# Performance work log

Measured on AMD Instinct MI355X. Metric: run time of the kernel, lower is better.

Reference implementation:

```python
import jax, jax.numpy as jnp
import numpy as np

N_NODES = 100000
N_EDGES = 3200000
IN_DIM = 128
H_GCN = 64
H_LSTM = 64


def setup_inputs() -> dict:
    key = jax.random.key(0)
    ks = jax.random.split(key, 12)
    s = 0.05
    return {
        "x": jax.random.normal(ks[0], (IN_DIM, N_NODES), dtype=jnp.float32),
        "edge_index": jax.random.randint(ks[1], (2, N_EDGES), 0, N_NODES, dtype=jnp.int32),
        "W1": jax.random.normal(ks[2], (IN_DIM, H_GCN), dtype=jnp.float32) * s,
        "b1": jnp.zeros((H_GCN,), dtype=jnp.float32),
        "W2": jax.random.normal(ks[3], (H_GCN, H_GCN), dtype=jnp.float32) * s,
        "b2": jnp.zeros((H_GCN,), dtype=jnp.float32),
        "w_ih": jax.random.normal(ks[4], (4 * H_LSTM, H_GCN), dtype=jnp.float32) * s,
        "w_hh": jax.random.normal(ks[5], (4 * H_LSTM, H_LSTM), dtype=jnp.float32) * s,
        "b_ih": jax.random.normal(ks[6], (4 * H_LSTM,), dtype=jnp.float32) * s,
        "b_hh": jax.random.normal(ks[7], (4 * H_LSTM,), dtype=jnp.float32) * s,
        "fc_w": jax.random.normal(ks[8], (1, H_LSTM), dtype=jnp.float32) * s,
        "fc_b": jnp.zeros((1,), dtype=jnp.float32),
    }


def gcn_conv(x, src, dst, n, W, b):
    # PyG GCNConv: add self loops, symmetric norm D^-1/2 (A+I) D^-1/2, linear-first.
    h = x @ W  # [N, out]
    loop = jnp.arange(n, dtype=src.dtype)
    s = jnp.concatenate([src, loop])
    d = jnp.concatenate([dst, loop])
    deg = jax.ops.segment_sum(jnp.ones(d.shape, dtype=h.dtype), d, num_segments=n)
    dinv = jnp.where(deg > 0, jax.lax.rsqrt(deg), 0.0)
    norm = dinv[s] * dinv[d]  # [E+N]
    out = jax.ops.segment_sum(h[s] * norm[:, None], d, num_segments=n)
    return out + b


def reference(x, edge_index, W1, b1, W2, b2, w_ih, w_hh, b_ih, b_hh, fc_w, fc_b):
    xt = x.T  # data.x.T -> [N, input_dim]
    n = xt.shape[0]
    src, dst = edge_index[0], edge_index[1]
    h = jax.nn.relu(gcn_conv(xt, src, dst, n, W1, b1))
    h = gcn_conv(h, src, dst, n, W2, b2)
    z = h[0][None, :]  # [1, H_GCN] node 0 embedding
    # single-step LSTM, zero initial state (h0=c0=0)
    gates = z @ w_ih.T + b_ih + b_hh  # [1, 4H]
    i, f, g, o = jnp.split(gates, 4, axis=-1)
    c = jax.nn.sigmoid(i) * jnp.tanh(g)  # f*c0 = 0
    hy = jax.nn.sigmoid(o) * jnp.tanh(c)  # [1, H_LSTM]
    y = hy @ fc_w.T + fc_b  # [1, 1]
    return y[:, :, None]  # [1, 1, 1]
```

## Files before the change

### kernel.cpp

```cpp
#include <hip/hip_runtime.h>
#include <math.h>

#define N_NODES 100000
#define N_EDGES 3200000
#define IN_DIM 128
#define HG 64

#define E0CAP 2048
#define MCAP  65536
#define NBMW  3125
#define SCAN_BLOCKS 1024
#define BLK_E0 16

#define OFF_DEG       0u
#define OFF_SLOTMAP   400000u
#define OFF_CNT       800000u
#define OFF_ACC       800032u
#define OFF_BMS1      1324320u
#define OFF_BMNEED    1336864u
#define WS_ZERO_BYTES 1349408u
#define OFF_BCNT      1349408u
#define OFF_BLIST     1353504u
#define OFF_EDGES0    1419040u
#define OFF_SLOTNODE  1427232u
#define OFF_MLISTS    1435424u
#define OFF_MLISTD    1697568u

__device__ __forceinline__ float dinv_of(int degv) {
    return 1.0f / sqrtf((float)(degv + 1));
}

__global__ void k_scan0(const int* __restrict__ src, const int* __restrict__ dst,
                        int4* __restrict__ zbase, int* __restrict__ bcnt,
                        int* __restrict__ blist) {
    __shared__ int lcnt;
    __shared__ int lsrc[BLK_E0];
    if (threadIdx.x == 0) lcnt = 0;
    __syncthreads();
    int tid = blockIdx.x * blockDim.x + threadIdx.x;
    int nth = gridDim.x * blockDim.x;
    const int nz = WS_ZERO_BYTES / 16;
    int4 z; z.x = 0; z.y = 0; z.z = 0; z.w = 0;
    for (int i = tid; i < nz; i += nth) zbase[i] = z;
    const int4* dst4 = (const int4*)dst;
    const int n4 = N_EDGES / 4;
    for (int i = tid; i < n4; i += nth) {
        int4 dv = dst4[i];
        int ds[4] = {dv.x, dv.y, dv.z, dv.w};
#pragma unroll
        for (int k = 0; k < 4; k++) {
            if (ds[k] == 0) {
                int p = atomicAdd(&lcnt, 1);
                if (p < BLK_E0) lsrc[p] = src[4 * i + k];
            }
        }
    }
    __syncthreads();
    int c = lcnt; if (c > BLK_E0) c = BLK_E0;
    if (threadIdx.x == 0) bcnt[blockIdx.x] = c;
    for (int i = threadIdx.x; i < c; i += blockDim.x)
        blist[blockIdx.x * BLK_E0 + i] = lsrc[i];
}

__global__ void k_build_slots(const int* __restrict__ bcnt, const int* __restrict__ blist,
                              int* __restrict__ edges0, int* __restrict__ slotnodes,
                              int* __restrict__ slotmap, int* __restrict__ cnt,
                              unsigned* __restrict__ bmS1) {
    const int t = threadIdx.x;
    for (int b = t; b < SCAN_BLOCKS; b += blockDim.x) {
        int c = bcnt[b];
        if (c > 0) {
            int p = atomicAdd(&cnt[0], c);
            for (int j = 0; j < c && p + j < E0CAP; j++)
                edges0[p + j] = blist[b * BLK_E0 + j];
        }
    }
    __syncthreads();
    int n0 = atomicAdd(&cnt[0], 0); if (n0 > E0CAP) n0 = E0CAP;
    for (int i = t; i < n0 + 1; i += blockDim.x) {
        int s = (i == n0) ? 0 : edges0[i];
        if (atomicCAS(&slotmap[s], 0, 1) == 0) {
            int p = atomicAdd(&cnt[1], 1);
            if (p < E0CAP) slotnodes[p] = s;
        }
    }
    __syncthreads();
    int ns = atomicAdd(&cnt[1], 0); if (ns > E0CAP) ns = E0CAP;
    for (int i = t; i < ns; i += blockDim.x) {
        int s = slotnodes[i];
        slotmap[s] = i + 1;
        atomicOr(&bmS1[s >> 5], 1u << (s & 31));
    }
}

__global__ void k_match(const int* __restrict__ src, const int* __restrict__ dst,
                        const int* __restrict__ slotmap,
                        const unsigned* __restrict__ bmS1, unsigned* __restrict__ bmNeed,
                        int* __restrict__ cnt, int* __restrict__ mlistS,
                        int* __restrict__ mlistD) {
    __shared__ unsigned sbm[NBMW];
    for (int i = threadIdx.x; i < NBMW; i += blockDim.x) sbm[i] = bmS1[i];
    __syncthreads();
    int tid = blockIdx.x * blockDim.x + threadIdx.x;
    int nth = gridDim.x * blockDim.x;
    const int4* dst4 = (const int4*)dst;
    const int n4 = N_EDGES / 4;
    for (int i = tid; i < n4; i += nth) {
        int4 dv = dst4[i];
        unsigned ds[4] = {(unsigned)dv.x, (unsigned)dv.y, (unsigned)dv.z, (unsigned)dv.w};
#pragma unroll
        for (int k = 0; k < 4; k++) {
            unsigned d = ds[k];
            if ((sbm[d >> 5] >> (d & 31)) & 1u) {
                int e = 4 * i + k;
                int s = src[e];
                int sl = slotmap[d] - 1;
                int p = atomicAdd(&cnt[2], 1);
                if (p < MCAP) {
                    mlistS[p] = s | (sl << 17);
                    mlistD[p] = (int)d;
                }
                atomicOr(&bmNeed[s >> 5], 1u << (s & 31));
            }
        }
    }
}

__global__ void k_deg_need(const int* __restrict__ dst, const unsigned* __restrict__ bmS1,
                           const unsigned* __restrict__ bmNeed, int* __restrict__ deg) {
    __shared__ unsigned sbm[NBMW];
    for (int i = threadIdx.x; i < NBMW; i += blockDim.x) sbm[i] = bmS1[i] | bmNeed[i];
    __syncthreads();
    int tid = blockIdx.x * blockDim.x + threadIdx.x;
    int nth = gridDim.x * blockDim.x;
    const int4* dst4 = (const int4*)dst;
    const int n4 = N_EDGES / 4;
    for (int i = tid; i < n4; i += nth) {
        int4 dv = dst4[i];
        unsigned ds[4] = {(unsigned)dv.x, (unsigned)dv.y, (unsigned)dv.z, (unsigned)dv.w};
#pragma unroll
        for (int k = 0; k < 4; k++) {
            unsigned d = ds[k];
            if ((sbm[d >> 5] >> (d & 31)) & 1u) atomicAdd(&deg[d], 1);
        }
    }
}

__global__ void k_contrib(const int* __restrict__ deg, const int* __restrict__ cnt,
                          const int* __restrict__ mlistS, const int* __restrict__ mlistD,
                          const int* __restrict__ slotnodes,
                          const float* __restrict__ x, const float* __restrict__ W1,
                          float* __restrict__ acc) {
    int m = cnt[2]; if (m > MCAP) m = MCAP;
    int ns = cnt[1]; if (ns > E0CAP) ns = E0CAP;
    const int vtotal = 2 * (m + ns);
    const int j = threadIdx.x;
    for (int v = blockIdx.x; v < vtotal; v += gridDim.x) {
        const int ii = v >> 1;
        const int kbase = (v & 1) << 6;
        int s, sl;
        float w;
        if (ii < m) {
            int sw = mlistS[ii];
            int d = mlistD[ii];
            s = sw & 0x1FFFF;
            sl = sw >> 17;
            w = dinv_of(deg[s]) * dinv_of(deg[d]);
        } else {
            sl = ii - m;
            s = slotnodes[sl];
            float dv = dinv_of(deg[s]);
            w = dv * dv;
        }
        const float* xp = x + (size_t)kbase * N_NODES + s;
        const float* wp = W1 + kbase * HG + j;
        float g = 0.f;
#pragma unroll
        for (int k = 0; k < 64; k++) {
            g = fmaf(xp[(size_t)k * N_NODES], wp[k * HG], g);
        }
        atomicAdd(&acc[sl * HG + j], g * w);
    }
}

#define CHUNK 256
__global__ void k_final(const float* __restrict__ b1, const float* __restrict__ W2,
                        const float* __restrict__ b2, const float* __restrict__ w_ih,
                        const float* __restrict__ b_ih, const float* __restrict__ b_hh,
                        const float* __restrict__ fc_w, const float* __restrict__ fc_b,
                        const int* __restrict__ deg, const int* __restrict__ slotmap,
                        const int* __restrict__ cnt, const int* __restrict__ edges0,
                        const float* __restrict__ acc, float* __restrict__ out) {
    __shared__ int   sh_sl[CHUNK];
    __shared__ float sh_w[CHUNK];
    __shared__ float partial[4][HG];
    __shared__ float agg[HG];
    __shared__ float zv[HG];
    __shared__ float gates[4 * HG];
    __shared__ float hw[HG];
    const int t = threadIdx.x;
    const int ch = t & (HG - 1);
    const int grp = t >> 6;
    int n0 = cnt[0]; if (n0 > E0CAP) n0 = E0CAP;

    const float dinv0 = dinv_of(deg[0]);
    const float bch = b1[ch];

    float a = 0.f;
    for (int base = 0; base < n0; base += CHUNK) {
        int cn = n0 - base; if (cn > CHUNK) cn = CHUNK;
        __syncthreads();
        if (t < cn) {
            int s = edges0[base + t];
            sh_sl[t] = slotmap[s] - 1;
            sh_w[t] = dinv_of(deg[s]) * dinv0;
        }
        __syncthreads();
        for (int i = grp; i < cn; i += 4) {
            float h = acc[sh_sl[i] * HG + ch] + bch;
            a = fmaf(sh_w[i], (h > 0.f ? h : 0.f), a);
        }
    }
    partial[grp][ch] = a;
    __syncthreads();
    if (t < HG) {
        int sl0 = slotmap[0] - 1;
        float h0 = acc[sl0 * HG + t] + b1[t];
        float s = dinv0 * dinv0 * (h0 > 0.f ? h0 : 0.f);
        s += partial[0][t] + partial[1][t] + partial[2][t] + partial[3][t];
        agg[t] = s;
    }
    __syncthreads();

    if (t < HG) {
        float zz = b2[t];
#pragma unroll 8
        for (int k = 0; k < HG; k++) zz = fmaf(agg[k], W2[k * HG + t], zz);
        zv[t] = zz;
    }
    __syncthreads();

    {
        float gt = b_ih[t] + b_hh[t];
#pragma unroll 8
        for (int jj = 0; jj < HG; jj++) gt = fmaf(zv[jj], w_ih[t * HG + jj], gt);
        gates[t] = gt;
    }
    __syncthreads();

    if (t < HG) {
        float ig = 1.f / (1.f + expf(-gates[t]));
        float gg = tanhf(gates[2 * HG + t]);
        float og = 1.f / (1.f + expf(-gates[3 * HG + t]));
        float c = ig * gg;
        float hy = og * tanhf(c);
        hw[t] = hy * fc_w[t];
    }
    __syncthreads();
    if (t == 0) {
        float y = fc_b[0];
        for (int jj = 0; jj < HG; jj++) y += hw[jj];
        out[0] = y;
    }
}

extern "C" void kernel_launch(void* const* d_in, const int* in_sizes, int n_in,
                              void* d_out, int out_size, void* d_ws, size_t ws_size,
                              hipStream_t stream) {
    const float* x    = (const float*)d_in[0];
    const int*   ei   = (const int*)d_in[1];
    const float* W1   = (const float*)d_in[2];
    const float* b1   = (const float*)d_in[3];
    const float* W2   = (const float*)d_in[4];
    const float* b2   = (const float*)d_in[5];
    const float* w_ih = (const float*)d_in[6];
    const float* b_ih = (const float*)d_in[8];
    const float* b_hh = (const float*)d_in[9];
    const float* fc_w = (const float*)d_in[10];
    const float* fc_b = (const float*)d_in[11];
    float* out = (float*)d_out;

    const int* src = ei;
    const int* dst = ei + N_EDGES;

    char* ws = (char*)d_ws;
    int*      deg       = (int*)(ws + OFF_DEG);
    int*      slotmap   = (int*)(ws + OFF_SLOTMAP);
    int*      cnt       = (int*)(ws + OFF_CNT);
    float*    acc       = (float*)(ws + OFF_ACC);
    unsigned* bmS1      = (unsigned*)(ws + OFF_BMS1);
    unsigned* bmNeed    = (unsigned*)(ws + OFF_BMNEED);
    int*      bcnt      = (int*)(ws + OFF_BCNT);
    int*      blist     = (int*)(ws + OFF_BLIST);
    int*      edges0    = (int*)(ws + OFF_EDGES0);
    int*      slotnodes = (int*)(ws + OFF_SLOTNODE);
    int*      mlistS    = (int*)(ws + OFF_MLISTS);
    int*      mlistD    = (int*)(ws + OFF_MLISTD);

    k_scan0<<<SCAN_BLOCKS, 256, 0, stream>>>(src, dst, (int4*)ws, bcnt, blist);
    k_build_slots<<<1, 256, 0, stream>>>(bcnt, blist, edges0, slotnodes, slotmap, cnt, bmS1);
    k_match<<<SCAN_BLOCKS, 256, 0, stream>>>(src, dst, slotmap, bmS1, bmNeed, cnt,
                                             mlistS, mlistD);
    k_deg_need<<<SCAN_BLOCKS, 256, 0, stream>>>(dst, bmS1, bmNeed, deg);
    k_contrib<<<4096, 64, 0, stream>>>(deg, cnt, mlistS, mlistD, slotnodes, x, W1, acc);
    k_final<<<1, 256, 0, stream>>>(b1, W2, b2, w_ih, b_ih, b_hh, fc_w, fc_b,
                                   deg, slotmap, cnt, edges0, acc, out);
}
```

Baseline: 170.6 us.

## Fuse six-kernel pipeline into one cooperative kernel with grid syncs

Merges the scan, slot-building, matching, degree counting, contribution and final LSTM stages into one cooperative kernel of 512x256 threads, with grid.sync between phases. The aim is to remove five kernel launch gaps and their inter-kernel drain/fill bubbles. The serial single-block stages now run while the rest of the grid waits at barriers. The scan also drops from 1024 to 512 blocks and the contrib phase from 4096 to 512. If the cooperative launch fails, the code falls back to the original six launches.

```diff
diff --git a/kernel.cpp b/kernel.cpp
--- a/kernel.cpp
+++ b/kernel.cpp
@@ -1,5 +1,8 @@
 #include <hip/hip_runtime.h>
+#include <hip/hip_cooperative_groups.h>
 #include <math.h>
+
+namespace cg = cooperative_groups;
 
 #define N_NODES 100000
 #define N_EDGES 3200000
@@ -11,6 +14,9 @@
 #define NBMW  3125
 #define SCAN_BLOCKS 1024
 #define BLK_E0 16
+
+#define NBLK 512
+#define NTHR 256
 
 #define OFF_DEG       0u
 #define OFF_SLOTMAP   400000u
@@ -26,8 +32,260 @@
 #define OFF_MLISTS    1435424u
 #define OFF_MLISTD    1697568u
 
+#define CHUNK 256
+
 __device__ __forceinline__ float dinv_of(int degv) {
     return 1.0f / sqrtf((float)(degv + 1));
+}
+
+__global__ void __launch_bounds__(NTHR, 2)
+k_fused(const int* __restrict__ src, const int* __restrict__ dst,
+        const float* __restrict__ x, const float* __restrict__ W1,
+        const float* __restrict__ b1, const float* __restrict__ W2,
+        const float* __restrict__ b2, const float* __restrict__ w_ih,
+        const float* __restrict__ b_ih, const float* __restrict__ b_hh,
+        const float* __restrict__ fc_w, const float* __restrict__ fc_b,
+        char* __restrict__ ws, float* __restrict__ out)
+{
+    int*      deg       = (int*)(ws + OFF_DEG);
+    int*      slotmap   = (int*)(ws + OFF_SLOTMAP);
+    int*      cnt       = (int*)(ws + OFF_CNT);
+    float*    acc       = (float*)(ws + OFF_ACC);
+    unsigned* bmS1      = (unsigned*)(ws + OFF_BMS1);
+    unsigned* bmNeed    = (unsigned*)(ws + OFF_BMNEED);
+    int*      bcnt      = (int*)(ws + OFF_BCNT);
+    int*      blist     = (int*)(ws + OFF_BLIST);
+    int*      edges0    = (int*)(ws + OFF_EDGES0);
+    int*      slotnodes = (int*)(ws + OFF_SLOTNODE);
+    int*      mlistS    = (int*)(ws + OFF_MLISTS);
+    int*      mlistD    = (int*)(ws + OFF_MLISTD);
+
+    cg::grid_group grid = cg::this_grid();
+
+    __shared__ unsigned sbm[NBMW];
+    __shared__ int lcnt;
+    __shared__ int lsrc[BLK_E0];
+    __shared__ int   sh_sl[CHUNK];
+    __shared__ float sh_w[CHUNK];
+    __shared__ float partial[4][HG];
+    __shared__ float aggv[HG];
+    __shared__ float zv[HG];
+    __shared__ float gates[4 * HG];
+    __shared__ float hw[HG];
+
+    const int bid = blockIdx.x;
+    const int t   = threadIdx.x;
+    const int tid = bid * NTHR + t;
+    const int nth = NBLK * NTHR;
+
+    if (t == 0) lcnt = 0;
+    __syncthreads();
+    {
+        int4 z; z.x = 0; z.y = 0; z.z = 0; z.w = 0;
+        int4* zb = (int4*)ws;
+        const int nz = WS_ZERO_BYTES / 16;
+        for (int i = tid; i < nz; i += nth) zb[i] = z;
+        const int4* dst4 = (const int4*)dst;
+        const int n4 = N_EDGES / 4;
+        for (int i = tid; i < n4; i += nth) {
+            int4 dv = dst4[i];
+            int ds[4] = {dv.x, dv.y, dv.z, dv.w};
+#pragma unroll
+            for (int k = 0; k < 4; k++) {
+                if (ds[k] == 0) {
+                    int p = atomicAdd(&lcnt, 1);
+                    if (p < BLK_E0) lsrc[p] = src[4 * i + k];
+                }
+            }
+        }
+    }
+    __syncthreads();
+    {
+        int c = lcnt; if (c > BLK_E0) c = BLK_E0;
+        if (t == 0) bcnt[bid] = c;
+        for (int i = t; i < c; i += NTHR) blist[bid * BLK_E0 + i] = lsrc[i];
+    }
+    __threadfence();
+    grid.sync();
+
+    if (bid == 0) {
+        for (int b = t; b < NBLK; b += NTHR) {
+            int c = bcnt[b];
+            if (c > 0) {
+                int p = atomicAdd(&cnt[0], c);
+                for (int j = 0; j < c && p + j < E0CAP; j++)
+                    edges0[p + j] = blist[b * BLK_E0 + j];
+            }
+        }
+        __syncthreads();
+        int n0 = atomicAdd(&cnt[0], 0); if (n0 > E0CAP) n0 = E0CAP;
+        for (int i = t; i < n0 + 1; i += NTHR) {
+            int s = (i == n0) ? 0 : edges0[i];
+            if (atomicCAS(&slotmap[s], 0, 1) == 0) {
+                int p = atomicAdd(&cnt[1], 1);
+                if (p < E0CAP) slotnodes[p] = s;
+            }
+        }
+        __syncthreads();
+        int ns = atomicAdd(&cnt[1], 0); if (ns > E0CAP) ns = E0CAP;
+        for (int i = t; i < ns; i += NTHR) {
+            int s = slotnodes[i];
+            slotmap[s] = i + 1;
+            atomicOr(&bmS1[s >> 5], 1u << (s & 31));
+        }
+    }
+    __threadfence();
+    grid.sync();
+
+    for (int i = t; i < NBMW; i += NTHR) sbm[i] = bmS1[i];
+    __syncthreads();
+    {
+        const int4* dst4 = (const int4*)dst;
+        const int n4 = N_EDGES / 4;
+        for (int i = tid; i < n4; i += nth) {
+            int4 dv = dst4[i];
+            unsigned ds[4] = {(unsigned)dv.x, (unsigned)dv.y,
+                              (unsigned)dv.z, (unsigned)dv.w};
+#pragma unroll
+            for (int k = 0; k < 4; k++) {
+                unsigned d = ds[k];
+                if ((sbm[d >> 5] >> (d & 31)) & 1u) {
+                    int e = 4 * i + k;
+                    int s = src[e];
+                    int sl = slotmap[d] - 1;
+                    int p = atomicAdd(&cnt[2], 1);
+                    if (p < MCAP) {
+                        mlistS[p] = s | (sl << 17);
+                        mlistD[p] = (int)d;
+                    }
+                    atomicOr(&bmNeed[s >> 5], 1u << (s & 31));
+                }
+            }
+        }
+    }
+    __threadfence();
+    grid.sync();
+
+    for (int i = t; i < NBMW; i += NTHR) sbm[i] |= bmNeed[i];
+    __syncthreads();
+    {
+        const int4* dst4 = (const int4*)dst;
+        const int n4 = N_EDGES / 4;
+        for (int i = tid; i < n4; i += nth) {
+            int4 dv = dst4[i];
+            unsigned ds[4] = {(unsigned)dv.x, (unsigned)dv.y,
+                              (unsigned)dv.z, (unsigned)dv.w};
+#pragma unroll
+            for (int k = 0; k < 4; k++) {
+                unsigned d = ds[k];
+                if ((sbm[d >> 5] >> (d & 31)) & 1u) atomicAdd(&deg[d], 1);
+            }
+        }
+    }
+    __threadfence();
+    grid.sync();
+
+    {
+        int m = cnt[2]; if (m > MCAP) m = MCAP;
+        int ns = cnt[1]; if (ns > E0CAP) ns = E0CAP;
+        const int vtotal = 2 * (m + ns);
+        const int j = t & 63;
+        const int grp = t >> 6;
+        for (int v = bid * 4 + grp; v < vtotal; v += NBLK * 4) {
+            const int ii = v >> 1;
+            const int kbase = (v & 1) << 6;
+            int s, sl;
+            float w;
+            if (ii < m) {
+                int sw = mlistS[ii];
+                int d = mlistD[ii];
+                s = sw & 0x1FFFF;
+                sl = sw >> 17;
+                w = dinv_of(deg[s]) * dinv_of(deg[d]);
+            } else {
+                sl = ii - m;
+                s = slotnodes[sl];
+                float dv = dinv_of(deg[s]);
+                w = dv * dv;
+            }
+            const float* xp = x + (size_t)kbase * N_NODES + s;
+            const float* wp = W1 + kbase * HG + j;
+            float g = 0.f;
+#pragma unroll
+            for (int k = 0; k < 64; k++) {
+                g = fmaf(xp[(size_t)k * N_NODES], wp[k * HG], g);
+            }
+            atomicAdd(&acc[sl * HG + j], g * w);
+        }
+    }
+    __threadfence();
+    grid.sync();
+
+    if (bid == 0) {
+        const int ch = t & (HG - 1);
+        const int grp = t >> 6;
+        int n0 = cnt[0]; if (n0 > E0CAP) n0 = E0CAP;
+
+        const float dinv0 = dinv_of(deg[0]);
+        const float bch = b1[ch];
+
+        float a = 0.f;
+        for (int base = 0; base < n0; base += CHUNK) {
+            int cn = n0 - base; if (cn > CHUNK) cn = CHUNK;
+            __syncthreads();
+            if (t < cn) {
+                int s = edges0[base + t];
+                sh_sl[t] = slotmap[s] - 1;
+                sh_w[t] = dinv_of(deg[s]) * dinv0;
+            }
+            __syncthreads();
+            for (int i = grp; i < cn; i += 4) {
+                float h = acc[sh_sl[i] * HG + ch] + bch;
+                a = fmaf(sh_w[i], (h > 0.f ? h : 0.f), a);
+            }
+        }
+        partial[grp][ch] = a;
+        __syncthreads();
+        if (t < HG) {
+            int sl0 = slotmap[0] - 1;
+            float h0 = acc[sl0 * HG + t] + b1[t];
+            float sg = dinv0 * dinv0 * (h0 > 0.f ? h0 : 0.f);
+            sg += partial[0][t] + partial[1][t] + partial[2][t] + partial[3][t];
+            aggv[t] = sg;
+        }
+        __syncthreads();
+
+        if (t < HG) {
+            float zz = b2[t];
+#pragma unroll 8
+            for (int k = 0; k < HG; k++) zz = fmaf(aggv[k], W2[k * HG + t], zz);
+            zv[t] = zz;
+        }
+        __syncthreads();
+
+        {
+            float gt = b_ih[t] + b_hh[t];
+#pragma unroll 8
+            for (int jj = 0; jj < HG; jj++) gt = fmaf(zv[jj], w_ih[t * HG + jj], gt);
+            gates[t] = gt;
+        }
+        __syncthreads();
+
+        if (t < HG) {
+            float ig = 1.f / (1.f + expf(-gates[t]));
+            float gg = tanhf(gates[2 * HG + t]);
+            float og = 1.f / (1.f + expf(-gates[3 * HG + t]));
+            float c = ig * gg;
+            float hy = og * tanhf(c);
+            hw[t] = hy * fc_w[t];
+        }
+        __syncthreads();
+        if (t == 0) {
+            float y = fc_b[0];
+            for (int jj = 0; jj < HG; jj++) y += hw[jj];
+            out[0] = y;
+        }
+    }
 }
 
 __global__ void k_scan0(const int* __restrict__ src, const int* __restrict__ dst,
@@ -183,7 +441,6 @@
     }
 }
 
-#define CHUNK 256
 __global__ void k_final(const float* __restrict__ b1, const float* __restrict__ W2,
                         const float* __restrict__ b2, const float* __restrict__ w_ih,
                         const float* __restrict__ b_ih, const float* __restrict__ b_hh,
@@ -282,27 +539,36 @@
 
     const int* src = ei;
     const int* dst = ei + N_EDGES;
-
     char* ws = (char*)d_ws;
-    int*      deg       = (int*)(ws + OFF_DEG);
-    int*      slotmap   = (int*)(ws + OFF_SLOTMAP);
-    int*      cnt       = (int*)(ws + OFF_CNT);
-    float*    acc       = (float*)(ws + OFF_ACC);
-    unsigned* bmS1      = (unsigned*)(ws + OFF_BMS1);
-    unsigned* bmNeed    = (unsigned*)(ws + OFF_BMNEED);
-    int*      bcnt      = (int*)(ws + OFF_BCNT);
-    int*      blist     = (int*)(ws + OFF_BLIST);
-    int*      edges0    = (int*)(ws + OFF_EDGES0);
-    int*      slotnodes = (int*)(ws + OFF_SLOTNODE);
-    int*      mlistS    = (int*)(ws + OFF_MLISTS);
-    int*      mlistD    = (int*)(ws + OFF_MLISTD);
-
-    k_scan0<<<SCAN_BLOCKS, 256, 0, stream>>>(src, dst, (int4*)ws, bcnt, blist);
-    k_build_slots<<<1, 256, 0, stream>>>(bcnt, blist, edges0, slotnodes, slotmap, cnt, bmS1);
-    k_match<<<SCAN_BLOCKS, 256, 0, stream>>>(src, dst, slotmap, bmS1, bmNeed, cnt,
-                                             mlistS, mlistD);
-    k_deg_need<<<SCAN_BLOCKS, 256, 0, stream>>>(dst, bmS1, bmNeed, deg);
-    k_contrib<<<4096, 64, 0, stream>>>(deg, cnt, mlistS, mlistD, slotnodes, x, W1, acc);
-    k_final<<<1, 256, 0, stream>>>(b1, W2, b2, w_ih, b_ih, b_hh, fc_w, fc_b,
-                                   deg, slotmap, cnt, edges0, acc, out);
-}
+
+    void* args[] = {(void*)&src, (void*)&dst, (void*)&x, (void*)&W1, (void*)&b1,
+                    (void*)&W2, (void*)&b2, (void*)&w_ih, (void*)&b_ih,
+                    (void*)&b_hh, (void*)&fc_w, (void*)&fc_b, (void*)&ws, (void*)&out};
+    hipError_t err = hipLaunchCooperativeKernel((const void*)k_fused, dim3(NBLK),
+                                                dim3(NTHR), args, 0, stream);
+
+    if (err != hipSuccess) {
+        int*      deg       = (int*)(ws + OFF_DEG);
+        int*      slotmap   = (int*)(ws + OFF_SLOTMAP);
+        int*      cnt       = (int*)(ws + OFF_CNT);
+        float*    acc       = (float*)(ws + OFF_ACC);
+        unsigned* bmS1      = (unsigned*)(ws + OFF_BMS1);
+        unsigned* bmNeed    = (unsigned*)(ws + OFF_BMNEED);
+        int*      bcnt      = (int*)(ws + OFF_BCNT);
+        int*      blist     = (int*)(ws + OFF_BLIST);
+        int*      edges0    = (int*)(ws + OFF_EDGES0);
+        int*      slotnodes = (int*)(ws + OFF_SLOTNODE);
+        int*      mlistS    = (int*)(ws + OFF_MLISTS);
+        int*      mlistD    = (int*)(ws + OFF_MLISTD);
+
+        k_scan0<<<SCAN_BLOCKS, 256, 0, stream>>>(src, dst, (int4*)ws, bcnt, blist);
+        k_build_slots<<<1, 256, 0, stream>>>(bcnt, blist, edges0, slotnodes, slotmap,
+                                             cnt, bmS1);
+        k_match<<<SCAN_BLOCKS, 256, 0, stream>>>(src, dst, slotmap, bmS1, bmNeed, cnt,
+                                                 mlistS, mlistD);
+        k_deg_need<<<SCAN_BLOCKS, 256, 0, stream>>>(dst, bmS1, bmNeed, deg);
+        k_contrib<<<4096, 64, 0, stream>>>(deg, cnt, mlistS, mlistD, slotnodes, x, W1, acc);
+        k_final<<<1, 256, 0, stream>>>(b1, W2, b2, w_ih, b_ih, b_hh, fc_w, fc_b,
+                                       deg, slotmap, cnt, edges0, acc, out);
+    }
+}
```

New measurement: 636.0 us. 3.73x slower.

## Fuse contrib and final kernels via last-block completion counter; shrink scan grids

Applied to the files above, without the earlier changes.

Merges the per-edge contribution kernel and the single-block final LSTM kernel into one launch. The last block to finish, detected with an atomic counter in cnt[3] after a threadfence, runs the tail computation. The contribution work now uses 256-thread blocks holding four 64-wide groups instead of 64-thread blocks, and the scan/match/degree kernels drop from 1024 to 256 blocks. This removes one kernel launch and its gap, at the cost of a grid-wide atomic handoff and lower parallelism in the scan kernels. It relies on cnt[3] being zeroed in the workspace clear.

```diff
diff --git a/kernel.cpp b/kernel.cpp
--- a/kernel.cpp
+++ b/kernel.cpp
@@ -9,8 +9,9 @@
 #define E0CAP 2048
 #define MCAP  65536
 #define NBMW  3125
-#define SCAN_BLOCKS 1024
+#define SCAN_BLOCKS 256
 #define BLK_E0 16
+#define CF_BLOCKS 1024
 
 #define OFF_DEG       0u
 #define OFF_SLOTMAP   400000u
@@ -25,6 +26,8 @@
 #define OFF_SLOTNODE  1427232u
 #define OFF_MLISTS    1435424u
 #define OFF_MLISTD    1697568u
+
+#define CHUNK 256
 
 __device__ __forceinline__ float dinv_of(int degv) {
     return 1.0f / sqrtf((float)(degv + 1));
@@ -146,59 +149,69 @@
     }
 }
 
-__global__ void k_contrib(const int* __restrict__ deg, const int* __restrict__ cnt,
-                          const int* __restrict__ mlistS, const int* __restrict__ mlistD,
-                          const int* __restrict__ slotnodes,
-                          const float* __restrict__ x, const float* __restrict__ W1,
-                          float* __restrict__ acc) {
-    int m = cnt[2]; if (m > MCAP) m = MCAP;
-    int ns = cnt[1]; if (ns > E0CAP) ns = E0CAP;
-    const int vtotal = 2 * (m + ns);
-    const int j = threadIdx.x;
-    for (int v = blockIdx.x; v < vtotal; v += gridDim.x) {
-        const int ii = v >> 1;
-        const int kbase = (v & 1) << 6;
-        int s, sl;
-        float w;
-        if (ii < m) {
-            int sw = mlistS[ii];
-            int d = mlistD[ii];
-            s = sw & 0x1FFFF;
-            sl = sw >> 17;
-            w = dinv_of(deg[s]) * dinv_of(deg[d]);
-        } else {
-            sl = ii - m;
-            s = slotnodes[sl];
-            float dv = dinv_of(deg[s]);
-            w = dv * dv;
-        }
-        const float* xp = x + (size_t)kbase * N_NODES + s;
-        const float* wp = W1 + kbase * HG + j;
-        float g = 0.f;
+__global__ void k_contrib_final(
+        const int* __restrict__ deg, const int* __restrict__ slotmap,
+        int* __restrict__ cnt,
+        const int* __restrict__ mlistS, const int* __restrict__ mlistD,
+        const int* __restrict__ slotnodes, const int* __restrict__ edges0,
+        const float* __restrict__ x, const float* __restrict__ W1,
+        const float* __restrict__ b1, const float* __restrict__ W2,
+        const float* __restrict__ b2, const float* __restrict__ w_ih,
+        const float* __restrict__ b_ih, const float* __restrict__ b_hh,
+        const float* __restrict__ fc_w, const float* __restrict__ fc_b,
+        float* __restrict__ acc, float* __restrict__ out) {
+    const int t = threadIdx.x;
+    {
+        int m = cnt[2]; if (m > MCAP) m = MCAP;
+        int ns = cnt[1]; if (ns > E0CAP) ns = E0CAP;
+        const int vtotal = 2 * (m + ns);
+        const int j = t & 63;
+        const int grp = t >> 6;
+        for (int v = blockIdx.x * 4 + grp; v < vtotal; v += CF_BLOCKS * 4) {
+            const int ii = v >> 1;
+            const int kbase = (v & 1) << 6;
+            int s, sl;
+            float w;
+            if (ii < m) {
+                int sw = mlistS[ii];
+                int d = mlistD[ii];
+                s = sw & 0x1FFFF;
+                sl = sw >> 17;
+                w = dinv_of(deg[s]) * dinv_of(deg[d]);
+            } else {
+                sl = ii - m;
+                s = slotnodes[sl];
+                float dv = dinv_of(deg[s]);
+                w = dv * dv;
+            }
+            const float* xp = x + (size_t)kbase * N_NODES + s;
+            const float* wp = W1 + kbase * HG + j;
+            float g = 0.f;
 #pragma unroll
-        for (int k = 0; k < 64; k++) {
-            g = fmaf(xp[(size_t)k * N_NODES], wp[k * HG], g);
-        }
-        atomicAdd(&acc[sl * HG + j], g * w);
-    }
-}
-
-#define CHUNK 256
-__global__ void k_final(const float* __restrict__ b1, const float* __restrict__ W2,
-                        const float* __restrict__ b2, const float* __restrict__ w_ih,
-                        const float* __restrict__ b_ih, const float* __restrict__ b_hh,
-                        const float* __restrict__ fc_w, const float* __restrict__ fc_b,
-                        const int* __restrict__ deg, const int* __restrict__ slotmap,
-                        const int* __restrict__ cnt, const int* __restrict__ edges0,
-                        const float* __restrict__ acc, float* __restrict__ out) {
+            for (int k = 0; k < 64; k++) {
+                g = fmaf(xp[(size_t)k * N_NODES], wp[k * HG], g);
+            }
+            atomicAdd(&acc[sl * HG + j], g * w);
+        }
+    }
+    __shared__ int amLast;
+    __threadfence();
+    __syncthreads();
+    if (t == 0) {
+        int prev = atomicAdd(&cnt[3], 1);
+        amLast = (prev == (int)gridDim.x - 1);
+    }
+    __syncthreads();
+    if (!amLast) return;
+    __threadfence();
+
     __shared__ int   sh_sl[CHUNK];
     __shared__ float sh_w[CHUNK];
     __shared__ float partial[4][HG];
-    __shared__ float agg[HG];
+    __shared__ float aggv[HG];
     __shared__ float zv[HG];
     __shared__ float gates[4 * HG];
     __shared__ float hw[HG];
-    const int t = threadIdx.x;
     const int ch = t & (HG - 1);
     const int grp = t >> 6;
     int n0 = cnt[0]; if (n0 > E0CAP) n0 = E0CAP;
@@ -226,16 +239,16 @@
     if (t < HG) {
         int sl0 = slotmap[0] - 1;
         float h0 = acc[sl0 * HG + t] + b1[t];
-        float s = dinv0 * dinv0 * (h0 > 0.f ? h0 : 0.f);
-        s += partial[0][t] + partial[1][t] + partial[2][t] + partial[3][t];
-        agg[t] = s;
+        float sg = dinv0 * dinv0 * (h0 > 0.f ? h0 : 0.f);
+        sg += partial[0][t] + partial[1][t] + partial[2][t] + partial[3][t];
+        aggv[t] = sg;
     }
     __syncthreads();
 
     if (t < HG) {
         float zz = b2[t];
 #pragma unroll 8
-        for (int k = 0; k < HG; k++) zz = fmaf(agg[k], W2[k * HG + t], zz);
+        for (int k = 0; k < HG; k++) zz = fmaf(aggv[k], W2[k * HG + t], zz);
         zv[t] = zz;
     }
     __syncthreads();
@@ -302,7 +315,7 @@
     k_match<<<SCAN_BLOCKS, 256, 0, stream>>>(src, dst, slotmap, bmS1, bmNeed, cnt,
                                              mlistS, mlistD);
     k_deg_need<<<SCAN_BLOCKS, 256, 0, stream>>>(dst, bmS1, bmNeed, deg);
-    k_contrib<<<4096, 64, 0, stream>>>(deg, cnt, mlistS, mlistD, slotnodes, x, W1, acc);
-    k_final<<<1, 256, 0, stream>>>(b1, W2, b2, w_ih, b_ih, b_hh, fc_w, fc_b,
-                                   deg, slotmap, cnt, edges0, acc, out);
-}
+    k_contrib_final<<<CF_BLOCKS, 256, 0, stream>>>(deg, slotmap, cnt, mlistS, mlistD,
+                                                   slotnodes, edges0, x, W1, b1, W2, b2,
+                                                   w_ih, b_ih, b_hh, fc_w, fc_b, acc, out);
+}
```

Measured after the change: 248.0 us. 1.45x slower.
